# Performance work log

Measured on AMD Instinct MI355X. Metric: run time of the kernel, lower is better.

The kernel has to match this reference:

```python
import math
import jax, jax.numpy as jnp
import numpy as np

B, S = 2, 2048
D, H, DK = 1024, 16, 64
M = 16            # nb_features
L = 4             # n_layers
DFF = 4096
VS, VT = 69, 69   # src/tgt vocab
NU = 10000        # num_users
FD = 34           # feature_dim
EPS = 1e-6


def make_pe(seq_len, d_model):
    pos = np.arange(seq_len, dtype=np.float32)[:, None]
    div = np.exp(np.arange(0, d_model, 2, dtype=np.float32) * (-math.log(10000.0) / d_model))
    pe = np.zeros((seq_len, d_model), np.float32)
    pe[:, 0::2] = np.sin(pos * div)
    pe[:, 1::2] = np.cos(pos * div)
    return jnp.asarray(pe)


def gelu_approx(x):
    return 0.5 * x * (1.0 + jnp.tanh(math.sqrt(2.0 / math.pi) * (x + 0.044715 * x ** 3)))


def layer_norm(x, alpha, bias):
    # torch LayerNormalization: unbiased std, eps added to std
    mu = x.mean(-1, keepdims=True)
    var = ((x - mu) ** 2).sum(-1, keepdims=True) / (x.shape[-1] - 1)
    return alpha * (x - mu) / (jnp.sqrt(var) + EPS) + bias


def setup_inputs():
    key = jax.random.key(0)
    ks = jax.random.split(key, 24)
    w = lambda k, shape, s=0.02: (jax.random.normal(k, shape, jnp.float32) * s)
    inp = {}
    inp['ids'] = jax.random.randint(ks[0], (B, S), 0, VS)
    inp['user_ids'] = jax.random.randint(ks[1], (B,), 0, NU)
    inp['id_embed'] = w(ks[2], (VS, D), 1.0)
    inp['feat_proj'] = w(ks[3], (D, FD))
    inp['gamma'] = jnp.float32(1.0)
    inp['gate_logits'] = w(ks[4], (NU, H))
    inp['wq'] = w(ks[5], (L, D, D))
    inp['wk'] = w(ks[6], (L, D, D))
    inp['wv'] = w(ks[7], (L, D, D))
    inp['wo'] = w(ks[8], (L, D, D))
    inp['omega'] = jax.random.normal(ks[9], (L, M, DK), jnp.float32) / math.sqrt(DK)
    inp['ln1_a'] = jnp.ones((L, D)); inp['ln1_b'] = jnp.zeros((L, D))
    inp['ln2_a'] = jnp.ones((L, D)); inp['ln2_b'] = jnp.zeros((L, D))
    inp['ff_w1'] = w(ks[10], (L, DFF, D)); inp['ff_b1'] = jnp.zeros((L, DFF))
    inp['ff_w2'] = w(ks[11], (L, D, DFF)); inp['ff_b2'] = jnp.zeros((L, D))
    inp['fin_a'] = jnp.ones((D,)); inp['fin_b'] = jnp.zeros((D,))
    inp['proj_w'] = w(ks[12], (VT, D)); inp['proj_b'] = jnp.zeros((VT,))
    inp['feat_tbl'] = w(ks[13], (VS, FD), 1.0)
    pm = np.zeros(VS, bool); pm[10:] = True   # ids >= 10 are products
    inp['prod_mask'] = jnp.asarray(pm)
    inp['pe'] = make_pe(S, D)
    return inp


def performer(xn, wq, wk, wv, wo, omega, gate):
    b, sq, _ = xn.shape
    q = (xn @ wq.T).reshape(b, sq, H, DK)
    k = (xn @ wk.T).reshape(b, sq, H, DK)
    v = (xn @ wv.T).reshape(b, sq, H, DK)
    # exp kernel feature map + row normalization
    qp = jnp.exp(-0.5 * (q @ omega.T) ** 2)        # (B,S,H,M)
    kp = jnp.exp(-0.5 * (k @ omega.T) ** 2)
    qp = qp / (qp.sum(-1, keepdims=True) + EPS)
    kp = kp / (kp.sum(-1, keepdims=True) + EPS)
    K_cum = jnp.cumsum(kp, axis=1)                              # (B,S,H,M)
    KV_cum = jnp.cumsum(kp[..., None] * v[..., None, :], axis=1)  # (B,S,H,M,DK)
    # blockwise causal index (block_size_h = block_size_w = 1)
    bh, bw = 1, 1
    ki = jnp.minimum((jnp.arange(sq) // bh + 1) * bw - 1, sq - 1)
    Ks = jnp.take(K_cum, ki, axis=1)
    KVs = jnp.take(KV_cum, ki, axis=1)
    num = jnp.einsum('bshm,bshmd->bshd', qp, KVs)
    den = jnp.sum(qp * Ks, -1, keepdims=True)
    out = num / (den + EPS)
    out = out * gate[:, None, :, None]
    return out.reshape(b, sq, D) @ wo.T


def reference(ids, user_ids, id_embed, feat_proj, gamma, gate_logits,
              wq, wk, wv, wo, omega, ln1_a, ln1_b, ln2_a, ln2_b,
              ff_w1, ff_b1, ff_w2, ff_b2, fin_a, fin_b,
              proj_w, proj_b, feat_tbl, prod_mask, pe):
    # SpecialPlusFeatureLookup
    id_vec = id_embed[ids]                       # (B,S,D)
    feat_vec = feat_tbl[ids] @ feat_proj.T       # (B,S,D)
    keep = prod_mask[ids]
    x = id_vec + gamma * (feat_vec * keep[..., None])
    # positional encoding (dropout=eval -> identity)
    x = x + pe[None, :x.shape[1], :]
    # per-user head gate
    gate = jax.nn.softmax(gate_logits[user_ids], axis=-1)  # (B,H)
    for l in range(L):
        x = x + performer(layer_norm(x, ln1_a[l], ln1_b[l]),
                          wq[l], wk[l], wv[l], wo[l], omega[l], gate)
        xn = layer_norm(x, ln2_a[l], ln2_b[l])
        x = x + (gelu_approx(xn @ ff_w1[l].T + ff_b1[l]) @ ff_w2[l].T + ff_b2[l])
    x = layer_norm(x, fin_a, fin_b)
    return x @ proj_w.T + proj_b                 # (B,S,VT)
```

## Files before the change

kernel.cpp:

```cpp
#include <hip/hip_runtime.h>
#include <hip/hip_bf16.h>
#include <math.h>

constexpr int BB  = 2;
constexpr int SS  = 2048;
constexpr int DD  = 1024;
constexpr int HH  = 16;
constexpr int DKK = 64;
constexpr int MB  = 16;
constexpr int LL  = 4;
constexpr int DF  = 4096;
constexpr int VSZ = 69;
constexpr int VTT = 69;
constexpr int FDD = 34;
constexpr float EPSF = 1e-6f;
constexpr int CL = 32;
constexpr int NC = SS / CL;

typedef unsigned short u16;
typedef unsigned int   u32;
using bf16x8 = __attribute__((ext_vector_type(8))) short;
using f32x4  = __attribute__((ext_vector_type(4))) float;

static __device__ __forceinline__ float b2f(u16 u) {
    union { u32 i; float f; } p; p.i = ((u32)u) << 16; return p.f;
}
static __device__ __forceinline__ u16 f2b(float f) {
    union { float f; u32 i; } p; p.f = f;
    u32 r = p.i + 0x7fffu + ((p.i >> 16) & 1u);
    return (u16)(r >> 16);
}
static __device__ __forceinline__ u32 pack2(float lo, float hi) {
    __hip_bfloat162 h = __float22bfloat162_rn(make_float2(lo, hi));
    return *(u32*)&h;
}
static __device__ __forceinline__ float gelu_f(float x) {
    float z = 0.7978845608028654f * (x + 0.044715f * x * x * x);
    z = fminf(fmaxf(z, -10.f), 10.f);
    float e = __expf(2.f * z);
    float th = (e - 1.f) / (e + 1.f);
    return 0.5f * x * (1.f + th);
}
static __device__ __forceinline__ float ldg1(const void* p, size_t i, int f32) {
    return f32 ? ((const float*)p)[i] : b2f(((const u16*)p)[i]);
}
static __device__ __forceinline__ float4 ldg4(const void* p, size_t i, int f32) {
    if (f32) return *(const float4*)((const float*)p + i);
    ushort4 u = *(const ushort4*)((const u16*)p + i);
    return make_float4(b2f(u.x), b2f(u.y), b2f(u.z), b2f(u.w));
}

#define GLD16(gp, lp) __builtin_amdgcn_global_load_lds( \
    (const __attribute__((address_space(1))) void*)(gp), \
    (__attribute__((address_space(3))) void*)(lp), 16, 0, 0)

__global__ void k_flag(const void* __restrict__ gamma, int* __restrict__ flag) {
    if (threadIdx.x == 0) *flag = (((const u16*)gamma)[0] == 0) ? 1 : 0;
}

__global__ __launch_bounds__(256) void k_build_tbl(
    const void* __restrict__ id_embed, const void* __restrict__ feat_tbl,
    const void* __restrict__ feat_proj, const void* __restrict__ gamma,
    const int* __restrict__ flagp, float* __restrict__ tbl)
{
    const int f32 = *flagp;
    int idx = blockIdx.x * 256 + threadIdx.x;
    if (idx >= VSZ * DD) return;
    int id = idx / DD, d = idx % DD;
    float acc = ldg1(id_embed, idx, f32);
    if (id >= 10) {
        float g = ldg1(gamma, 0, f32);
        float s = 0.f;
        for (int f = 0; f < FDD; ++f)
            s += ldg1(feat_tbl, (size_t)id * FDD + f, f32) * ldg1(feat_proj, (size_t)d * FDD + f, f32);
        acc += g * s;
    }
    tbl[idx] = acc;
}

__global__ __launch_bounds__(256) void k_gather(
    const float* __restrict__ tbl, const int* __restrict__ ids,
    const void* __restrict__ pe, const int* __restrict__ flagp, float* __restrict__ x)
{
    const int f32 = *flagp;
    int idx = blockIdx.x * 256 + threadIdx.x;
    int bs = idx >> 10, d = idx & (DD - 1);
    int s = bs & (SS - 1);
    x[idx] = tbl[ids[bs] * DD + d] + ldg1(pe, (size_t)s * DD + d, f32);
}

__global__ void k_gate(const void* __restrict__ gl, const int* __restrict__ uid,
                       const int* __restrict__ flagp, float* __restrict__ gate)
{
    const int f32 = *flagp;
    int b = threadIdx.x;
    if (b >= BB) return;
    size_t off = (size_t)uid[b] * HH;
    float v[HH], mx = -1e30f;
    for (int i = 0; i < HH; ++i) { v[i] = ldg1(gl, off + i, f32); mx = fmaxf(mx, v[i]); }
    float s = 0.f;
    for (int i = 0; i < HH; ++i) { v[i] = expf(v[i] - mx); s += v[i]; }
    for (int i = 0; i < HH; ++i) gate[b * HH + i] = v[i] / s;
}

__global__ __launch_bounds__(256) void k_layernorm(
    const float* __restrict__ x, const void* __restrict__ alpha,
    const void* __restrict__ beta, size_t p_off,
    const int* __restrict__ flagp, u16* __restrict__ y)
{
    const int f32 = *flagp;
    int row = blockIdx.x;
    const float* xr = x + (size_t)row * DD;
    int t = threadIdx.x;
    float v[4]; float s = 0.f;
    #pragma unroll
    for (int j = 0; j < 4; ++j) { v[j] = xr[t + j * 256]; s += v[j]; }
    __shared__ float red[8];
    int lane = t & 63, wv = t >> 6;
    #pragma unroll
    for (int off = 32; off > 0; off >>= 1) s += __shfl_down(s, off, 64);
    if (lane == 0) red[wv] = s;
    __syncthreads();
    float mu = (red[0] + red[1] + red[2] + red[3]) * (1.f / DD);
    __syncthreads();
    float ss = 0.f;
    #pragma unroll
    for (int j = 0; j < 4; ++j) { float dv = v[j] - mu; ss += dv * dv; }
    #pragma unroll
    for (int off = 32; off > 0; off >>= 1) ss += __shfl_down(ss, off, 64);
    if (lane == 0) red[wv] = ss;
    __syncthreads();
    float var = (red[0] + red[1] + red[2] + red[3]) * (1.f / (DD - 1));
    float rs = 1.f / (sqrtf(var) + EPSF);
    u16* yr = y + (size_t)row * DD;
    #pragma unroll
    for (int j = 0; j < 4; ++j) {
        int d = t + j * 256;
        yr[d] = f2b(ldg1(alpha, p_off + d, f32) * (v[j] - mu) * rs + ldg1(beta, p_off + d, f32));
    }
}

template<int BN, int BK>
static __device__ __forceinline__ void gemm_core(
    const u16* __restrict__ A, int lda,
    const void* __restrict__ W, size_t w_off, int ldw,
    const void* __restrict__ bias, size_t b_off, int f32,
    int K, int O, int act, int mode, u16* __restrict__ Cb, float* __restrict__ resid,
    int bx, int by)
{
    constexpr int NP  = BK / 32;
    constexpr int NI  = (BN == 128) ? 4 : 2;
    constexpr int WCOLS = (BN == 128) ? 4 : 2;
    __shared__ u16 As[NP * 64 * 32];
    __shared__ u16 Bs[NP * BN * 32];
    int t = threadIdx.x;
    int lane = t & 63, w = t >> 6;
    int quad = lane >> 4, l16 = lane & 15;
    int wm = (w / WCOLS) * (NI * 16);
    int wn = (w % WCOLS) * 32;
    int n0 = by * 64, o0 = bx * BN;

    f32x4 acc[NI][2];
    #pragma unroll
    for (int i = 0; i < NI; ++i)
        #pragma unroll
        for (int j = 0; j < 2; ++j)
            #pragma unroll
            for (int r = 0; r < 4; ++r) acc[i][j][r] = 0.f;

    int r0 = t >> 2, c0 = (t & 3) * 8;
    const u16* Ap = A + (size_t)n0 * lda + c0;
    char* AsB = (char*)As;
    char* BsB = (char*)Bs;

    for (int k0 = 0; k0 < K; k0 += BK) {
        #pragma unroll
        for (int p = 0; p < NP; ++p) {
            int kk = k0 + p * 32;
            char* AsP = AsB + p * 4096;
            char* BsP = BsB + p * (BN * 64);
            GLD16(Ap + (size_t)r0 * lda + kk, AsP + t * 16);
            if (f32) {
                const float* Wf = (const float*)W + w_off + kk + c0;
                const float* q0 = Wf + (size_t)(o0 + r0) * ldw;
                float4 xa = *(const float4*)q0, xb = *(const float4*)(q0 + 4);
                uint4 pk;
                pk.x = pack2(xa.x, xa.y); pk.y = pack2(xa.z, xa.w);
                pk.z = pack2(xb.x, xb.y); pk.w = pack2(xb.z, xb.w);
                *(uint4*)(BsP + t * 16) = pk;
                if (BN == 128) {
                    const float* q1 = q0 + (size_t)64 * ldw;
                    float4 ya = *(const float4*)q1, yb = *(const float4*)(q1 + 4);
                    pk.x = pack2(ya.x, ya.y); pk.y = pack2(ya.z, ya.w);
                    pk.z = pack2(yb.x, yb.y); pk.w = pack2(yb.z, yb.w);
                    *(uint4*)(BsP + 4096 + t * 16) = pk;
                }
            } else {
                const u16* Wb = (const u16*)W + w_off + kk + c0;
                GLD16(Wb + (size_t)(o0 + r0) * ldw, BsP + t * 16);
                if (BN == 128)
                    GLD16(Wb + (size_t)(o0 + r0 + 64) * ldw, BsP + 4096 + t * 16);
            }
        }
        __syncthreads();
        #pragma unroll
        for (int p = 0; p < NP; ++p) {
            const u16* AsP = As + p * (64 * 32);
            const u16* BsP = Bs + p * (BN * 32);
            bf16x8 af[NI], bfv[2];
            #pragma unroll
            for (int i = 0; i < NI; ++i)
                af[i] = *(const bf16x8*)(AsP + (size_t)(wm + i * 16 + l16) * 32 + quad * 8);
            #pragma unroll
            for (int j = 0; j < 2; ++j)
                bfv[j] = *(const bf16x8*)(BsP + (size_t)(wn + j * 16 + l16) * 32 + quad * 8);
            #pragma unroll
            for (int i = 0; i < NI; ++i)
                #pragma unroll
                for (int j = 0; j < 2; ++j)
                    acc[i][j] = __builtin_amdgcn_mfma_f32_16x16x32_bf16(af[i], bfv[j], acc[i][j], 0, 0, 0);
        }
        __syncthreads();
    }
    #pragma unroll
    for (int i = 0; i < NI; ++i) {
        #pragma unroll
        for (int j = 0; j < 2; ++j) {
            int col = o0 + wn + j * 16 + l16;
            float bval = bias ? ldg1(bias, b_off + col, f32) : 0.f;
            #pragma unroll
            for (int r = 0; r < 4; ++r) {
                int row = n0 + wm + i * 16 + quad * 4 + r;
                float val = acc[i][j][r] + bval;
                if (act) val = gelu_f(val);
                size_t idx = (size_t)row * O + col;
                if (mode == 1) resid[idx] += val;
                else           Cb[idx] = f2b(val);
            }
        }
    }
}

static __device__ __forceinline__ void xcd_tile(int& bx, int& by) {
    int gx = gridDim.x;
    int nwg = gx * gridDim.y;
    int h = blockIdx.y * gx + blockIdx.x;
    int q = nwg >> 3;
    int lid = (h & 7) * q + (h >> 3);
    bx = lid % gx; by = lid / gx;
}

__global__ __launch_bounds__(256) void k_gemm_a(
    const u16* __restrict__ A, int lda, const void* __restrict__ W, size_t w_off, int ldw,
    const void* __restrict__ bias, size_t b_off, const int* __restrict__ flagp,
    int K, int O, int act, int mode, u16* __restrict__ Cb, float* __restrict__ resid)
{
    int bx, by; xcd_tile(bx, by);
    gemm_core<128, 64>(A, lda, W, w_off, ldw, bias, b_off, *flagp, K, O, act, mode, Cb, resid,
                       bx, by);
}

__global__ __launch_bounds__(256) void k_gemm_b(
    const u16* __restrict__ A, int lda, const void* __restrict__ W, size_t w_off, int ldw,
    const void* __restrict__ bias, size_t b_off, const int* __restrict__ flagp,
    int K, int O, int act, int mode, u16* __restrict__ Cb, float* __restrict__ resid)
{
    int bx, by; xcd_tile(bx, by);
    gemm_core<64, 128>(A, lda, W, w_off, ldw, bias, b_off, *flagp, K, O, act, mode, Cb, resid,
                       bx, by);
}

__global__ __launch_bounds__(256) void k_gemm_qkv(
    const u16* __restrict__ A,
    const void* __restrict__ Wq, const void* __restrict__ Wk, const void* __restrict__ Wv,
    size_t w_off, const int* __restrict__ flagp,
    u16* __restrict__ oq, u16* __restrict__ ok, u16* __restrict__ ov)
{
    const void* W = (blockIdx.z == 0) ? Wq : (blockIdx.z == 1) ? Wk : Wv;
    u16* o = (blockIdx.z == 0) ? oq : (blockIdx.z == 1) ? ok : ov;
    int bx, by; xcd_tile(bx, by);
    gemm_core<128, 64>(A, DD, W, w_off, DD, nullptr, 0, *flagp, DD, DD, 0, 0, o, nullptr,
                       bx, by);
}

__global__ __launch_bounds__(256) void k_gemm_small(
    const u16* __restrict__ A, const void* __restrict__ W, size_t w_off, int ldw,
    const void* __restrict__ bias, size_t b_off,
    const int* __restrict__ flagp, int K, int O, void* __restrict__ outp)
{
    const int f32 = *flagp;
    __shared__ float As[16][68];
    __shared__ float Ws[16][68];
    int t = threadIdx.x;
    int tx = t & 15, ty = t >> 4;
    int o0 = blockIdx.x * 64, n0 = blockIdx.y * 64;
    int lr = t >> 2;
    int lk = (t & 3) * 4;
    float c[4][4] = {};
    for (int k0 = 0; k0 < K; k0 += 16) {
        ushort4 av = *(const ushort4*)(A + (size_t)(n0 + lr) * K + k0 + lk);
        As[lk + 0][lr] = b2f(av.x); As[lk + 1][lr] = b2f(av.y);
        As[lk + 2][lr] = b2f(av.z); As[lk + 3][lr] = b2f(av.w);
        float4 wv4 = make_float4(0.f, 0.f, 0.f, 0.f);
        int orow = o0 + lr;
        if (orow < O) wv4 = ldg4(W, w_off + (size_t)orow * ldw + k0 + lk, f32);
        Ws[lk + 0][lr] = wv4.x; Ws[lk + 1][lr] = wv4.y;
        Ws[lk + 2][lr] = wv4.z; Ws[lk + 3][lr] = wv4.w;
        __syncthreads();
        #pragma unroll
        for (int kk = 0; kk < 16; ++kk) {
            float4 a = *(const float4*)&As[kk][ty * 4];
            float4 b = *(const float4*)&Ws[kk][tx * 4];
            c[0][0] += a.x * b.x; c[0][1] += a.x * b.y; c[0][2] += a.x * b.z; c[0][3] += a.x * b.w;
            c[1][0] += a.y * b.x; c[1][1] += a.y * b.y; c[1][2] += a.y * b.z; c[1][3] += a.y * b.w;
            c[2][0] += a.z * b.x; c[2][1] += a.z * b.y; c[2][2] += a.z * b.z; c[2][3] += a.z * b.w;
            c[3][0] += a.w * b.x; c[3][1] += a.w * b.y; c[3][2] += a.w * b.z; c[3][3] += a.w * b.w;
        }
        __syncthreads();
    }
    #pragma unroll
    for (int i = 0; i < 4; ++i) {
        int n = n0 + ty * 4 + i;
        #pragma unroll
        for (int j = 0; j < 4; ++j) {
            int o = o0 + tx * 4 + j;
            if (o >= O) continue;
            float val = c[i][j];
            if (bias) val += ldg1(bias, b_off + o, f32);
            size_t idx = (size_t)n * O + o;
            if (f32) ((float*)outp)[idx] = val;
            else     ((u16*)outp)[idx] = f2b(val);
        }
    }
}

__global__ __launch_bounds__(256) void k_featmap(
    const u16* __restrict__ q, const void* __restrict__ omega, size_t o_off,
    const int* __restrict__ flagp, u16* __restrict__ qp_t)
{
    const int f32 = *flagp;
    __shared__ float q_s[64][68];
    __shared__ float om_s[16][68];
    int t = threadIdx.x;
    int bh = blockIdx.y, b = bh >> 4, h = bh & 15;
    int s0 = blockIdx.x * 64;
    const u16* qbase = q + (size_t)(b * SS + s0) * DD + h * DKK;
    #pragma unroll
    for (int i = 0; i < 2; ++i) {
        int idx = i * 256 + t;
        int si = idx >> 3, part = idx & 7;
        uint4 raw = *(const uint4*)(qbase + (size_t)si * DD + part * 8);
        const u16* pr = (const u16*)&raw;
        *(float4*)&q_s[si][part * 8]     = make_float4(b2f(pr[0]), b2f(pr[1]), b2f(pr[2]), b2f(pr[3]));
        *(float4*)&q_s[si][part * 8 + 4] = make_float4(b2f(pr[4]), b2f(pr[5]), b2f(pr[6]), b2f(pr[7]));
    }
    #pragma unroll
    for (int i = 0; i < 4; ++i) {
        int idx = i * 256 + t;
        om_s[idx >> 6][idx & 63] = ldg1(omega, o_off + idx, f32);
    }
    __syncthreads();
    int s = t >> 2, mg = t & 3;
    float u[4] = {0.f, 0.f, 0.f, 0.f};
    #pragma unroll
    for (int dk = 0; dk < 64; dk += 4) {
        float4 q4 = *(const float4*)&q_s[s][dk];
        #pragma unroll
        for (int mj = 0; mj < 4; ++mj) {
            float4 o4 = *(const float4*)&om_s[mg * 4 + mj][dk];
            u[mj] += q4.x * o4.x + q4.y * o4.y + q4.z * o4.z + q4.w * o4.w;
        }
    }
    float phi[4], tot = 0.f;
    #pragma unroll
    for (int mj = 0; mj < 4; ++mj) { phi[mj] = expf(-0.5f * u[mj] * u[mj]); tot += phi[mj]; }
    tot += __shfl_xor(tot, 1); tot += __shfl_xor(tot, 2);
    float inv = 1.f / (tot + EPSF);
    uint2 out;
    out.x = pack2(phi[0] * inv, phi[1] * inv);
    out.y = pack2(phi[2] * inv, phi[3] * inv);
    *(uint2*)(qp_t + ((size_t)bh * SS + s0 + s) * MB + mg * 4) = out;
}

__global__ __launch_bounds__(64) void k_scan_part(
    const u16* __restrict__ kp_t, const u16* __restrict__ v,
    float* __restrict__ kv_tot, float* __restrict__ kc_tot)
{
    int c = blockIdx.x, bh = blockIdx.y;
    int b = bh >> 4, h = bh & 15;
    int d = threadIdx.x;
    __shared__ float kp_s[CL * MB];
    const u16* kpb = kp_t + ((size_t)bh * SS + c * CL) * MB;
    #pragma unroll
    for (int i = 0; i < CL * MB / 64; ++i) {
        int idx = i * 64 + d;
        kp_s[idx] = b2f(kpb[idx]);
    }
    __syncthreads();
    float Kc[MB], KV[MB];
    #pragma unroll
    for (int m = 0; m < MB; ++m) { Kc[m] = 0.f; KV[m] = 0.f; }
    const u16* vp = v + ((size_t)b * SS + c * CL) * DD + h * DKK + d;
    for (int si = 0; si < CL; ++si) {
        float vd = b2f(vp[(size_t)si * DD]);
        #pragma unroll
        for (int m = 0; m < MB; ++m) {
            float kp = kp_s[si * MB + m];
            Kc[m] += kp; KV[m] += kp * vd;
        }
    }
    float* kvp = kv_tot + (((size_t)bh * NC + c) * MB) * DKK + d;
    #pragma unroll
    for (int m = 0; m < MB; ++m) kvp[(size_t)m * DKK] = KV[m];
    #pragma unroll
    for (int m = 0; m < MB; ++m)
        if (d == m) kc_tot[((size_t)bh * NC + c) * MB + m] = Kc[m];
}

__global__ __launch_bounds__(64) void k_scan_off(
    float* __restrict__ kv_tot, float* __restrict__ kc_tot)
{
    int bh = blockIdx.x; int d = threadIdx.x;
    if (d < MB) {
        float run = 0.f;
        for (int c = 0; c < NC; ++c) {
            size_t i = ((size_t)bh * NC + c) * MB + d;
            float tt = kc_tot[i]; kc_tot[i] = run; run += tt;
        }
    }
    float run[MB];
    #pragma unroll
    for (int m = 0; m < MB; ++m) run[m] = 0.f;
    for (int c = 0; c < NC; ++c) {
        size_t base = (((size_t)bh * NC + c) * MB) * DKK + d;
        float tt[MB];
        #pragma unroll
        for (int m = 0; m < MB; ++m) tt[m] = kv_tot[base + (size_t)m * DKK];
        #pragma unroll
        for (int m = 0; m < MB; ++m) { kv_tot[base + (size_t)m * DKK] = run[m]; run[m] += tt[m]; }
    }
}

__global__ __launch_bounds__(64) void k_scan_out(
    const u16* __restrict__ qp_t, const u16* __restrict__ kp_t, const u16* __restrict__ v,
    const float* __restrict__ kv_tot, const float* __restrict__ kc_tot,
    const float* __restrict__ gate, u16* __restrict__ attn)
{
    int c = blockIdx.x, bh = blockIdx.y;
    int b = bh >> 4, h = bh & 15;
    int d = threadIdx.x;
    __shared__ float kp_s[CL * MB], qp_s[CL * MB];
    const u16* kpb = kp_t + ((size_t)bh * SS + c * CL) * MB;
    const u16* qpb = qp_t + ((size_t)bh * SS + c * CL) * MB;
    #pragma unroll
    for (int i = 0; i < CL * MB / 64; ++i) {
        int idx = i * 64 + d;
        kp_s[idx] = b2f(kpb[idx]);
        qp_s[idx] = b2f(qpb[idx]);
    }
    __syncthreads();
    float Kc[MB], KV[MB];
    const float* kvp = kv_tot + (((size_t)bh * NC + c) * MB) * DKK + d;
    const float* kcp = kc_tot + ((size_t)bh * NC + c) * MB;
    #pragma unroll
    for (int m = 0; m < MB; ++m) { KV[m] = kvp[(size_t)m * DKK]; Kc[m] = kcp[m]; }
    float g = gate[bh];
    const u16* vp = v + ((size_t)b * SS + c * CL) * DD + h * DKK + d;
    u16* ap = attn + ((size_t)b * SS + c * CL) * DD + h * DKK + d;
    for (int si = 0; si < CL; ++si) {
        float vd = b2f(vp[(size_t)si * DD]);
        float num = 0.f, den = 0.f;
        #pragma unroll
        for (int m = 0; m < MB; ++m) {
            float kp = kp_s[si * MB + m];
            Kc[m] += kp; KV[m] += kp * vd;
            float qp = qp_s[si * MB + m];
            num += qp * KV[m]; den += qp * Kc[m];
        }
        ap[(size_t)si * DD] = f2b(num / (den + EPSF) * g);
    }
}

extern "C" void kernel_launch(void* const* d_in, const int* in_sizes, int n_in,
                              void* d_out, int out_size, void* d_ws, size_t ws_size,
                              hipStream_t stream)
{
    const int*  ids       = (const int*)d_in[0];
    const int*  user_ids  = (const int*)d_in[1];
    const void* id_embed  = d_in[2];
    const void* feat_proj = d_in[3];
    const void* gamma     = d_in[4];
    const void* gate_log  = d_in[5];
    const void* wq        = d_in[6];
    const void* wk        = d_in[7];
    const void* wv        = d_in[8];
    const void* wo        = d_in[9];
    const void* omega     = d_in[10];
    const void* ln1_a     = d_in[11];
    const void* ln1_b     = d_in[12];
    const void* ln2_a     = d_in[13];
    const void* ln2_b     = d_in[14];
    const void* ff_w1     = d_in[15];
    const void* ff_b1     = d_in[16];
    const void* ff_w2     = d_in[17];
    const void* ff_b2     = d_in[18];
    const void* fin_a     = d_in[19];
    const void* fin_b     = d_in[20];
    const void* proj_w    = d_in[21];
    const void* proj_b    = d_in[22];
    const void* feat_tbl  = d_in[23];
    const void* pe        = d_in[25];

    char* base = (char*)d_ws;
    const size_t MiB = (size_t)1 << 20;
    int*   flagp  = (int*)base;
    float* gate   = (float*)(base + 64);
    float* kc_tot = (float*)(base + 4096);
    float* tbl    = (float*)(base + 256 * 1024);
    float* x      = (float*)(base + 1 * MiB);
    u16*   xn     = (u16*)  (base + 17 * MiB);
    float* kv_tot = (float*)(base + 17 * MiB);
    u16*   qb     = (u16*)  (base + 25 * MiB);
    u16*   kb     = (u16*)  (base + 33 * MiB);
    u16*   vb     = (u16*)  (base + 41 * MiB);
    u16*   qp_t   = (u16*)  (base + 49 * MiB);
    u16*   kp_t   = (u16*)  (base + 51 * MiB);
    u16*   attn   = qb;
    u16*   ff1c   = qb;

    const int NT = BB * SS;

    k_flag<<<1, 64, 0, stream>>>(gamma, flagp);
    k_build_tbl<<<(VSZ * DD + 255) / 256, 256, 0, stream>>>(id_embed, feat_tbl, feat_proj, gamma, flagp, tbl);
    k_gather<<<(NT * DD) / 256, 256, 0, stream>>>(tbl, ids, pe, flagp, x);
    k_gate<<<1, 64, 0, stream>>>(gate_log, user_ids, flagp, gate);

    dim3 gQKV(DD / 128, NT / 64, 3);
    dim3 gWo(DD / 64, NT / 64);
    dim3 gF1(2048 / 128, NT / 64);
    dim3 gF2(DD / 64, NT / 64);
    dim3 gFeat(SS / 64, BB * HH);
    dim3 gScan(NC, BB * HH);

    for (int l = 0; l < LL; ++l) {
        size_t lDD = (size_t)l * DD * DD;
        k_layernorm<<<NT, 256, 0, stream>>>(x, ln1_a, ln1_b, (size_t)l * DD, flagp, xn);
        k_gemm_qkv<<<gQKV, 256, 0, stream>>>(xn, wq, wk, wv, lDD, flagp, qb, kb, vb);
        k_featmap<<<gFeat, 256, 0, stream>>>(qb, omega, (size_t)l * MB * DKK, flagp, qp_t);
        k_featmap<<<gFeat, 256, 0, stream>>>(kb, omega, (size_t)l * MB * DKK, flagp, kp_t);
        k_scan_part<<<gScan, 64, 0, stream>>>(kp_t, vb, kv_tot, kc_tot);
        k_scan_off<<<BB * HH, 64, 0, stream>>>(kv_tot, kc_tot);
        k_scan_out<<<gScan, 64, 0, stream>>>(qp_t, kp_t, vb, kv_tot, kc_tot, gate, attn);
        k_gemm_b<<<gWo, 256, 0, stream>>>(attn, DD, wo, lDD, DD, nullptr, 0, flagp, DD, DD, 0, 1, nullptr, x);
        k_layernorm<<<NT, 256, 0, stream>>>(x, ln2_a, ln2_b, (size_t)l * DD, flagp, xn);
        for (int c = 0; c < 2; ++c) {
            size_t w1_off = (size_t)l * DF * DD + (size_t)c * 2048 * DD;
            size_t b1_off = (size_t)l * DF + c * 2048;
            size_t w2_off = (size_t)l * DD * DF + (size_t)c * 2048;
            k_gemm_a<<<gF1, 256, 0, stream>>>(xn, DD, ff_w1, w1_off, DD, ff_b1, b1_off, flagp, DD, 2048, 1, 0, ff1c, nullptr);
            k_gemm_b<<<gF2, 256, 0, stream>>>(ff1c, 2048, ff_w2, w2_off, DF,
                                              (c == 0) ? ff_b2 : nullptr, (size_t)l * DD,
                                              flagp, 2048, DD, 0, 1, nullptr, x);
        }
    }
    k_layernorm<<<NT, 256, 0, stream>>>(x, fin_a, fin_b, 0, flagp, xn);
    dim3 g4((VTT + 63) / 64, NT / 64);
    k_gemm_small<<<g4, 256, 0, stream>>>(xn, proj_w, 0, DD, proj_b, 0, flagp, DD, VTT, d_out);
}
```

Measured before the change: 1.797 ms.

## Swizzle GEMM LDS layout and merge FFN chunks into single z-batched launches

Applies an XOR swizzle to the k-column chunk each thread loads and reads in LDS, to cut bank conflicts on the MFMA fragment reads. When the workspace is large enough, the two FFN halves run as one launch each (grid z=2) instead of four sequential launches. The FF1 output is written as a full 4096-wide bf16 buffer, and FF2 accumulates its two K-halves into the residual with atomicAdd. This gives more parallel work per launch but adds float atomics, which make the summation order nondeterministic, and it needs a larger scratch buffer.

```diff
diff --git a/kernel.cpp b/kernel.cpp
--- a/kernel.cpp
+++ b/kernel.cpp
@@ -168,8 +168,13 @@
             #pragma unroll
             for (int r = 0; r < 4; ++r) acc[i][j][r] = 0.f;
 
-    int r0 = t >> 2, c0 = (t & 3) * 8;
-    const u16* Ap = A + (size_t)n0 * lda + c0;
+    int r0 = t >> 2;
+    int swzt = (t >> 3) & 3;
+    int c0  = (t & 3) * 8;
+    int c0s = ((t & 3) ^ swzt) * 8;
+    int tsw = ((t & ~3) | ((t & 3) ^ swzt));
+    int quadx = quad ^ ((l16 >> 1) & 3);
+    const u16* Ap = A + (size_t)n0 * lda + c0s;
     char* AsB = (char*)As;
     char* BsB = (char*)Bs;
 
@@ -187,16 +192,16 @@
                 uint4 pk;
                 pk.x = pack2(xa.x, xa.y); pk.y = pack2(xa.z, xa.w);
                 pk.z = pack2(xb.x, xb.y); pk.w = pack2(xb.z, xb.w);
-                *(uint4*)(BsP + t * 16) = pk;
+                *(uint4*)(BsP + tsw * 16) = pk;
                 if (BN == 128) {
                     const float* q1 = q0 + (size_t)64 * ldw;
                     float4 ya = *(const float4*)q1, yb = *(const float4*)(q1 + 4);
                     pk.x = pack2(ya.x, ya.y); pk.y = pack2(ya.z, ya.w);
                     pk.z = pack2(yb.x, yb.y); pk.w = pack2(yb.z, yb.w);
-                    *(uint4*)(BsP + 4096 + t * 16) = pk;
+                    *(uint4*)(BsP + 4096 + tsw * 16) = pk;
                 }
             } else {
-                const u16* Wb = (const u16*)W + w_off + kk + c0;
+                const u16* Wb = (const u16*)W + w_off + kk + c0s;
                 GLD16(Wb + (size_t)(o0 + r0) * ldw, BsP + t * 16);
                 if (BN == 128)
                     GLD16(Wb + (size_t)(o0 + r0 + 64) * ldw, BsP + 4096 + t * 16);
@@ -210,10 +215,10 @@
             bf16x8 af[NI], bfv[2];
             #pragma unroll
             for (int i = 0; i < NI; ++i)
-                af[i] = *(const bf16x8*)(AsP + (size_t)(wm + i * 16 + l16) * 32 + quad * 8);
+                af[i] = *(const bf16x8*)(AsP + (size_t)(wm + i * 16 + l16) * 32 + quadx * 8);
             #pragma unroll
             for (int j = 0; j < 2; ++j)
-                bfv[j] = *(const bf16x8*)(BsP + (size_t)(wn + j * 16 + l16) * 32 + quad * 8);
+                bfv[j] = *(const bf16x8*)(BsP + (size_t)(wn + j * 16 + l16) * 32 + quadx * 8);
             #pragma unroll
             for (int i = 0; i < NI; ++i)
                 #pragma unroll
@@ -234,8 +239,9 @@
                 float val = acc[i][j][r] + bval;
                 if (act) val = gelu_f(val);
                 size_t idx = (size_t)row * O + col;
-                if (mode == 1) resid[idx] += val;
-                else           Cb[idx] = f2b(val);
+                if (mode == 1)      resid[idx] += val;
+                else if (mode == 2) atomicAdd(&resid[idx], val);
+                else                Cb[idx] = f2b(val);
             }
         }
     }
@@ -281,6 +287,30 @@
     int bx, by; xcd_tile(bx, by);
     gemm_core<128, 64>(A, DD, W, w_off, DD, nullptr, 0, *flagp, DD, DD, 0, 0, o, nullptr,
                        bx, by);
+}
+
+__global__ __launch_bounds__(256) void k_gemm_ff1(
+    const u16* __restrict__ A, const void* __restrict__ W, size_t l_off_w,
+    const void* __restrict__ bias, size_t l_off_b, const int* __restrict__ flagp,
+    u16* __restrict__ Cb)
+{
+    int c = blockIdx.z;
+    int bx, by; xcd_tile(bx, by);
+    gemm_core<128, 64>(A, DD, W, l_off_w + (size_t)c * 2048 * DD, DD,
+                       bias, l_off_b + (size_t)c * 2048, *flagp,
+                       DD, DF, 1, 0, Cb + (size_t)c * 2048, nullptr, bx, by);
+}
+
+__global__ __launch_bounds__(256) void k_gemm_ff2(
+    const u16* __restrict__ A, const void* __restrict__ W, size_t l_off_w,
+    const void* __restrict__ bias, size_t l_off_b, const int* __restrict__ flagp,
+    float* __restrict__ resid)
+{
+    int c = blockIdx.z;
+    int bx, by; xcd_tile(bx, by);
+    gemm_core<64, 128>(A + (size_t)c * 2048, DF, W, l_off_w + (size_t)c * 2048, DF,
+                       (c == 0) ? bias : nullptr, l_off_b, *flagp,
+                       2048, DD, 0, 2, nullptr, resid, bx, by);
 }
 
 __global__ __launch_bounds__(256) void k_gemm_small(
@@ -527,6 +557,8 @@
     u16*   kp_t   = (u16*)  (base + 51 * MiB);
     u16*   attn   = qb;
     u16*   ff1c   = qb;
+    u16*   ff1f   = qb;
+    const bool merged_ffn = (ws_size >= 57 * MiB);
 
     const int NT = BB * SS;
 
@@ -537,6 +569,8 @@
 
     dim3 gQKV(DD / 128, NT / 64, 3);
     dim3 gWo(DD / 64, NT / 64);
+    dim3 gF1m(2048 / 128, NT / 64, 2);
+    dim3 gF2m(DD / 64, NT / 64, 2);
     dim3 gF1(2048 / 128, NT / 64);
     dim3 gF2(DD / 64, NT / 64);
     dim3 gFeat(SS / 64, BB * HH);
@@ -553,14 +587,21 @@
         k_scan_out<<<gScan, 64, 0, stream>>>(qp_t, kp_t, vb, kv_tot, kc_tot, gate, attn);
         k_gemm_b<<<gWo, 256, 0, stream>>>(attn, DD, wo, lDD, DD, nullptr, 0, flagp, DD, DD, 0, 1, nullptr, x);
         k_layernorm<<<NT, 256, 0, stream>>>(x, ln2_a, ln2_b, (size_t)l * DD, flagp, xn);
-        for (int c = 0; c < 2; ++c) {
-            size_t w1_off = (size_t)l * DF * DD + (size_t)c * 2048 * DD;
-            size_t b1_off = (size_t)l * DF + c * 2048;
-            size_t w2_off = (size_t)l * DD * DF + (size_t)c * 2048;
-            k_gemm_a<<<gF1, 256, 0, stream>>>(xn, DD, ff_w1, w1_off, DD, ff_b1, b1_off, flagp, DD, 2048, 1, 0, ff1c, nullptr);
-            k_gemm_b<<<gF2, 256, 0, stream>>>(ff1c, 2048, ff_w2, w2_off, DF,
-                                              (c == 0) ? ff_b2 : nullptr, (size_t)l * DD,
-                                              flagp, 2048, DD, 0, 1, nullptr, x);
+        if (merged_ffn) {
+            k_gemm_ff1<<<gF1m, 256, 0, stream>>>(xn, ff_w1, (size_t)l * DF * DD, ff_b1,
+                                                 (size_t)l * DF, flagp, ff1f);
+            k_gemm_ff2<<<gF2m, 256, 0, stream>>>(ff1f, ff_w2, (size_t)l * DD * DF, ff_b2,
+                                                 (size_t)l * DD, flagp, x);
+        } else {
+            for (int c = 0; c < 2; ++c) {
+                size_t w1_off = (size_t)l * DF * DD + (size_t)c * 2048 * DD;
+                size_t b1_off = (size_t)l * DF + c * 2048;
+                size_t w2_off = (size_t)l * DD * DF + (size_t)c * 2048;
+                k_gemm_a<<<gF1, 256, 0, stream>>>(xn, DD, ff_w1, w1_off, DD, ff_b1, b1_off, flagp, DD, 2048, 1, 0, ff1c, nullptr);
+                k_gemm_b<<<gF2, 256, 0, stream>>>(ff1c, 2048, ff_w2, w2_off, DF,
+                                                  (c == 0) ? ff_b2 : nullptr, (size_t)l * DD,
+                                                  flagp, 2048, DD, 0, 1, nullptr, x);
+            }
         }
     }
     k_layernorm<<<NT, 256, 0, stream>>>(x, fin_a, fin_b, 0, flagp, xn);
```

After: 1.785 ms. Within noise of the previous version (-0.7%).
